# Performance work log

Measured on AMD Instinct MI355X. Metric: run time of the kernel, lower is better.

Reference implementation:

```python
import jax, jax.numpy as jnp
import numpy as np

B, S, H, NH = 2, 2048, 1024, 16
DH = H // NH  # 64

def setup_inputs() -> dict:
    key = jax.random.key(0)
    ks = jax.random.split(key, 6)
    return {
        "hidden_states": jax.random.normal(ks[0], (B, S, H), jnp.float32),
        "attention_mask": jnp.zeros((B, 1, 1, S), jnp.float32),  # additive mask (0 = attend)
        "local_attention_mask": jax.random.randint(ks[1], (B, 1, S, S), 0, 2).astype(jnp.int32),
        "gate_outputs": jax.random.uniform(ks[2], (B, NH, S, 1), jnp.float32),
        "Wq": jax.random.normal(ks[3], (H, H), jnp.float32) * 0.02,
        "bq": jnp.zeros((H,), jnp.float32),
        "Wk": jax.random.normal(ks[4], (H, H), jnp.float32) * 0.02,
        "bk": jnp.zeros((H,), jnp.float32),
        "Wv": jax.random.normal(ks[5], (H, H), jnp.float32) * 0.02,
        "bv": jnp.zeros((H,), jnp.float32),
    }

def _heads(x):
    # [B,S,H] -> [B,NH,S,DH]
    return x.reshape(B, S, NH, DH).transpose(0, 2, 1, 3)

def reference(hidden_states, attention_mask, local_attention_mask, gate_outputs, Wq, bq, Wk, bk, Wv, bv):
    q = _heads(hidden_states @ Wq.T + bq)
    k = _heads(hidden_states @ Wk.T + bk)
    v = _heads(hidden_states @ Wv.T + bv)
    scores = jnp.einsum("bhqd,bhkd->bhqk", q, k) / jnp.sqrt(jnp.float32(DH))
    # global branch (additive mask)
    probs_g = jax.nn.softmax(scores + attention_mask, axis=-1)
    ctx_g = jnp.einsum("bhqk,bhkd->bhqd", probs_g, v)
    # local branch: 0/1 mask -> additive -inf mask
    lmask = (1.0 - local_attention_mask.astype(jnp.float32)) * jnp.finfo(jnp.float32).min
    probs_l = jax.nn.softmax(scores + lmask, axis=-1)
    ctx_l = jnp.einsum("bhqk,bhkd->bhqd", probs_l, v)
    ctx = gate_outputs * ctx_l + (1.0 - gate_outputs) * ctx_g  # [B,NH,S,DH]
    return ctx.transpose(0, 2, 1, 3).reshape(B, S, H)
```

## Files before the change

kernel.cpp:

```cpp
#include <hip/hip_runtime.h>
#include <cstdint>
#include <cstddef>

typedef short short8 __attribute__((ext_vector_type(8)));
typedef short short4v __attribute__((ext_vector_type(4)));
typedef float floatx4 __attribute__((ext_vector_type(4)));
typedef unsigned short ushort4v __attribute__((ext_vector_type(4)));

constexpr int B_ = 2, S_ = 2048, H_ = 1024, NH_ = 16, DH_ = 64;
constexpr int K_ = H_;

__device__ __forceinline__ unsigned short f2bf(float f) {
  unsigned u = __float_as_uint(f);
  u += 0x7fffu + ((u >> 16) & 1u);
  return (unsigned short)(u >> 16);
}

__device__ __forceinline__ unsigned pack2bf(float a, float b) {
  unsigned ua = (__float_as_uint(a) + 0x8000u) >> 16;
  unsigned ub = (__float_as_uint(b) + 0x8000u) & 0xffff0000u;
  return ua | ub;
}

__global__ __launch_bounds__(256) void prep_kernel(
    const float* __restrict__ hs, unsigned short* __restrict__ hbf,
    const float* __restrict__ Wq, const float* __restrict__ Wk, const float* __restrict__ Wv,
    unsigned short* __restrict__ wqb, unsigned short* __restrict__ wkb,
    unsigned short* __restrict__ wvb,
    const int* __restrict__ lm, unsigned long long* __restrict__ bm,
    const float* __restrict__ am, float* __restrict__ ea) {
  const int bid = blockIdx.x, tid = threadIdx.x;
  if (bid < 7168) {
    const float* in;
    unsigned short* out;
    int off;
    if (bid < 4096) { in = hs; out = hbf; off = bid; }
    else {
      int wsel = (bid - 4096) >> 10;
      in = (wsel == 0) ? Wq : (wsel == 1) ? Wk : Wv;
      out = (wsel == 0) ? wqb : (wsel == 1) ? wkb : wvb;
      off = (bid - 4096) & 1023;
    }
    int i = (off * 256 + tid) * 4;
    float4 v = *reinterpret_cast<const float4*>(in + i);
    ushort4v o;
    o.x = f2bf(v.x); o.y = f2bf(v.y); o.z = f2bf(v.z); o.w = f2bf(v.w);
    *reinterpret_cast<ushort4v*>(out + i) = o;
  } else if (bid < 39936) {
    int word = (bid - 7168) * 4 + (tid >> 6);
    int lane = tid & 63;
    unsigned long long bits = __ballot(lm[(size_t)word * 64 + lane] != 0);
    if (lane == 0) bm[word] = bits;
  } else {
    int i = (bid - 39936) * 256 + tid;
    ea[i] = __expf(am[i]);
  }
}

typedef __attribute__((address_space(1))) const void gvoid;
typedef __attribute__((address_space(3))) void lvoid;
__device__ __forceinline__ void async16(const unsigned short* gp, unsigned short* lp) {
  __builtin_amdgcn_global_load_lds((gvoid*)gp, (lvoid*)lp, 16, 0, 0);
}

__global__ __launch_bounds__(256) void gemm_qkv(
    const unsigned short* __restrict__ A,
    const unsigned short* __restrict__ Wq, const unsigned short* __restrict__ Wk,
    const unsigned short* __restrict__ Wv,
    const float* __restrict__ bq, const float* __restrict__ bk, const float* __restrict__ bv,
    unsigned short* __restrict__ qo, unsigned short* __restrict__ ko,
    unsigned short* __restrict__ vo) {
  __shared__ alignas(16) unsigned short As[128 * 32];
  __shared__ alignas(16) unsigned short Bs[128 * 32];
  const int z = blockIdx.z;
  const unsigned short* W = (z == 0) ? Wq : (z == 1) ? Wk : Wv;
  const float* bias = (z == 0) ? bq : (z == 1) ? bk : bv;

  const int m0 = blockIdx.x * 128, n0 = blockIdx.y * 128;
  const int tid = threadIdx.x, lane = tid & 63, wvi = tid >> 6;
  const int wr = wvi >> 1, wc = wvi & 1, quad = lane >> 4, l16 = lane & 15;

  floatx4 zf = {0.f, 0.f, 0.f, 0.f};
  floatx4 acc[4][4];
  for (int i = 0; i < 4; i++)
    for (int j = 0; j < 4; j++) acc[i][j] = zf;

  for (int kk = 0; kk < K_; kk += 32) {
#pragma unroll
    for (int i = 0; i < 2; i++) {
      int cb = wvi * 128 + i * 64;
      int c = cb + lane;
      int row = c >> 2, kc = c & 3;
      async16(A + (size_t)(m0 + row) * K_ + kk + kc * 8, As + cb * 8);
      async16(W + (size_t)(n0 + row) * K_ + kk + kc * 8, Bs + cb * 8);
    }
    __syncthreads();
    short8 af[4], bfr[4];
#pragma unroll
    for (int mf = 0; mf < 4; mf++)
      af[mf] = *reinterpret_cast<const short8*>(&As[(wr * 64 + mf * 16 + l16) * 32 + quad * 8]);
#pragma unroll
    for (int nf = 0; nf < 4; nf++)
      bfr[nf] = *reinterpret_cast<const short8*>(&Bs[(wc * 64 + nf * 16 + l16) * 32 + quad * 8]);
    if (z == 2) {
#pragma unroll
      for (int mf = 0; mf < 4; mf++)
#pragma unroll
        for (int nf = 0; nf < 4; nf++)
          acc[mf][nf] = __builtin_amdgcn_mfma_f32_16x16x32_bf16(af[mf], bfr[nf], acc[mf][nf], 0, 0, 0);
    } else {
#pragma unroll
      for (int mf = 0; mf < 4; mf++)
#pragma unroll
        for (int nf = 0; nf < 4; nf++)
          acc[mf][nf] = __builtin_amdgcn_mfma_f32_16x16x32_bf16(bfr[nf], af[mf], acc[mf][nf], 0, 0, 0);
    }
    __syncthreads();
  }

  if (z == 2) {
#pragma unroll
    for (int mf = 0; mf < 4; mf++) {
      int mbase = m0 + wr * 64 + mf * 16 + quad * 4;
      int b = mbase >> 11, s0 = mbase & 2047;
#pragma unroll
      for (int nf = 0; nf < 4; nf++) {
        int n = n0 + wc * 64 + nf * 16 + l16;
        int h = n >> 6, d = n & 63;
        int bh = b * NH_ + h;
        float bvv = bias[n];
        floatx4 c = acc[mf][nf];
        size_t base = (size_t)bh * 131072 + (s0 >> 6) * 4096 + (d >> 4) * 1024 +
                      ((s0 >> 4) & 3) * 256 + ((s0 >> 2) & 3) * 64 + (d & 15) * 4;
        ushort4v p;
        p.x = f2bf(c[0] + bvv); p.y = f2bf(c[1] + bvv);
        p.z = f2bf(c[2] + bvv); p.w = f2bf(c[3] + bvv);
        *reinterpret_cast<ushort4v*>(&vo[base]) = p;
      }
    }
  } else {
#pragma unroll
    for (int mf = 0; mf < 4; mf++) {
      int s = m0 + wr * 64 + mf * 16 + l16;
      int b = s >> 11;
      int sq = s & 2047;
#pragma unroll
      for (int nf = 0; nf < 4; nf++) {
        int nn = n0 + wc * 64 + nf * 16 + quad * 4;
        int h = nn >> 6, dh = nn & 63;
        int bh = b * NH_ + h;
        float4 b4 = *reinterpret_cast<const float4*>(bias + nn);
        floatx4 c = acc[mf][nf];
        if (z == 0) {
          ushort4v p;
          p.x = f2bf((c[0] + b4.x) * 0.18033688011112042f);
          p.y = f2bf((c[1] + b4.y) * 0.18033688011112042f);
          p.z = f2bf((c[2] + b4.z) * 0.18033688011112042f);
          p.w = f2bf((c[3] + b4.w) * 0.18033688011112042f);
          *reinterpret_cast<ushort4v*>(&qo[((size_t)bh * S_ + sq) * DH_ + dh]) = p;
        } else {
          size_t base = (size_t)bh * 131072 + (sq >> 6) * 4096 + ((sq >> 4) & 3) * 1024 +
                        (dh >> 5) * 512 + ((dh >> 3) & 3) * 128 + (sq & 15) * 8 + (dh & 7);
          ushort4v p;
          p.x = f2bf(c[0] + b4.x); p.y = f2bf(c[1] + b4.y);
          p.z = f2bf(c[2] + b4.z); p.w = f2bf(c[3] + b4.w);
          *reinterpret_cast<ushort4v*>(&ko[base]) = p;
        }
      }
    }
  }
}

__global__ __launch_bounds__(256, 4) void attn_kernel(
    const unsigned short* __restrict__ q,
    const unsigned short* __restrict__ kperm,
    const unsigned short* __restrict__ vperm,
    const float* __restrict__ eam,
    const unsigned long long* __restrict__ bm,
    const float* __restrict__ gate,
    float* __restrict__ out) {
  __shared__ alignas(16) unsigned short Ks[2][4096];
  __shared__ alignas(16) unsigned short Vs[2][4096];

  const int flat = blockIdx.x;
  const int h = (flat & 7) + 8 * ((flat >> 3) & 1);
  const int b = (flat >> 4) & 1;
  const int qt = flat >> 5;
  const int tid = threadIdx.x, lane = tid & 63, wvi = tid >> 6;
  const int quad = lane >> 4, l16 = lane & 15;
  const int bh = b * NH_ + h;
  const int q0 = qt * 64 + wvi * 16;

  const unsigned short* qrow = q + ((size_t)bh * S_ + q0 + l16) * DH_;
  short8 qf0 = *reinterpret_cast<const short8*>(qrow + quad * 8);
  short8 qf1 = *reinterpret_cast<const short8*>(qrow + 32 + quad * 8);

  floatx4 zf = {0.f, 0.f, 0.f, 0.f};
  float psg = 0.f, psl = 0.f;
  floatx4 accg[4], accl[4];
#pragma unroll
  for (int i = 0; i < 4; i++) { accg[i] = zf; accl[i] = zf; }

  const unsigned short* kp = kperm + (size_t)bh * 131072;
  const unsigned short* vp = vperm + (size_t)bh * 131072;
  const float* eamb = eam + (size_t)b * S_;
  const unsigned long long* bmq = bm + ((size_t)b * S_ + q0 + l16) * (S_ / 64);

  const int soA = tid * 8, soB = 2048 + tid * 8;
  const unsigned short* kgA = kp + soA;
  const unsigned short* kgB = kp + soB;
  const unsigned short* vgA = vp + soA;
  const unsigned short* vgB = vp + soB;

  uint4 pk0 = *reinterpret_cast<const uint4*>(kgA);
  uint4 pk1 = *reinterpret_cast<const uint4*>(kgB);
  uint4 pv0 = *reinterpret_cast<const uint4*>(vgA);
  uint4 pv1 = *reinterpret_cast<const uint4*>(vgB);
  *reinterpret_cast<uint4*>(&Ks[0][soA]) = pk0;
  *reinterpret_cast<uint4*>(&Ks[0][soB]) = pk1;
  *reinterpret_cast<uint4*>(&Vs[0][soA]) = pv0;
  *reinterpret_cast<uint4*>(&Vs[0][soB]) = pv1;
  pk0 = *reinterpret_cast<const uint4*>(kgA + 4096);
  pk1 = *reinterpret_cast<const uint4*>(kgB + 4096);
  pv0 = *reinterpret_cast<const uint4*>(vgA + 4096);
  pv1 = *reinterpret_cast<const uint4*>(vgB + 4096);

  for (int kt = 0; kt < S_ / 64; kt++) {
    __syncthreads();
    {
      const int bn = (kt + 1) & 1;
      *reinterpret_cast<uint4*>(&Ks[bn][soA]) = pk0;
      *reinterpret_cast<uint4*>(&Ks[bn][soB]) = pk1;
      *reinterpret_cast<uint4*>(&Vs[bn][soA]) = pv0;
      *reinterpret_cast<uint4*>(&Vs[bn][soB]) = pv1;
    }
    {
      const int tb = ((kt + 2) & 31) * 4096;
      pk0 = *reinterpret_cast<const uint4*>(kgA + tb);
      pk1 = *reinterpret_cast<const uint4*>(kgB + tb);
      pv0 = *reinterpret_cast<const uint4*>(vgA + tb);
      pv1 = *reinterpret_cast<const uint4*>(vgB + tb);
    }
    const int k0 = kt * 64;
    unsigned long long w = bmq[kt];
    float4 ea[4];
#pragma unroll
    for (int t = 0; t < 4; t++)
      ea[t] = *reinterpret_cast<const float4*>(eamb + k0 + t * 16 + quad * 4);

    const unsigned short* Kc = Ks[kt & 1];
    const unsigned short* Vc = Vs[kt & 1];
    floatx4 scT[4];
#pragma unroll
    for (int t = 0; t < 4; t++) {
      const unsigned short* kr = Kc + t * 1024 + lane * 8;
      short8 kf0 = *reinterpret_cast<const short8*>(kr);
      short8 kf1 = *reinterpret_cast<const short8*>(kr + 512);
      scT[t] = __builtin_amdgcn_mfma_f32_16x16x32_bf16(kf0, qf0, zf, 0, 0, 0);
      scT[t] = __builtin_amdgcn_mfma_f32_16x16x32_bf16(kf1, qf1, scT[t], 0, 0, 0);
    }
    int pgf[4][2], plf[4][2];
#pragma unroll
    for (int t = 0; t < 4; t++) {
      unsigned m4 = (unsigned)(w >> (t * 16 + quad * 4)) & 0xFu;
      float e0 = __builtin_amdgcn_exp2f(scT[t][0]);
      float e1 = __builtin_amdgcn_exp2f(scT[t][1]);
      float e2 = __builtin_amdgcn_exp2f(scT[t][2]);
      float e3 = __builtin_amdgcn_exp2f(scT[t][3]);
      float g0 = e0 * ea[t].x, g1 = e1 * ea[t].y, g2 = e2 * ea[t].z, g3 = e3 * ea[t].w;
      psg += (g0 + g1) + (g2 + g3);
      float l0 = (m4 & 1u) ? e0 : 0.f;
      float l1 = (m4 & 2u) ? e1 : 0.f;
      float l2 = (m4 & 4u) ? e2 : 0.f;
      float l3 = (m4 & 8u) ? e3 : 0.f;
      psl += (l0 + l1) + (l2 + l3);
      pgf[t][0] = pack2bf(g0, g1); pgf[t][1] = pack2bf(g2, g3);
      plf[t][0] = pack2bf(l0, l1); plf[t][1] = pack2bf(l2, l3);
    }
#pragma unroll
    for (int d = 0; d < 4; d++) {
#pragma unroll
      for (int t = 0; t < 4; t++) {
        short4v vf = *reinterpret_cast<const short4v*>(Vc + d * 1024 + t * 256 + lane * 4);
        short4v pg = *reinterpret_cast<const short4v*>(&pgf[t][0]);
        short4v pl = *reinterpret_cast<const short4v*>(&plf[t][0]);
        accg[d] = __builtin_amdgcn_mfma_f32_16x16x16bf16_1k(vf, pg, accg[d], 0, 0, 0);
        accl[d] = __builtin_amdgcn_mfma_f32_16x16x16bf16_1k(vf, pl, accl[d], 0, 0, 0);
      }
    }
  }

  float lgf = psg;
  lgf += __shfl_xor(lgf, 16, 64);
  lgf += __shfl_xor(lgf, 32, 64);
  float llf = psl;
  llf += __shfl_xor(llf, 16, 64);
  llf += __shfl_xor(llf, 32, 64);
  const int s = q0 + l16;
  const float g = gate[(size_t)bh * S_ + s];
  const float cg = (1.f - g) / lgf, cl = g / llf;
  float* orow = out + ((size_t)b * S_ + s) * H_ + h * DH_ + quad * 4;
#pragma unroll
  for (int d = 0; d < 4; d++) {
    float4 o;
    o.x = cl * accl[d][0] + cg * accg[d][0];
    o.y = cl * accl[d][1] + cg * accg[d][1];
    o.z = cl * accl[d][2] + cg * accg[d][2];
    o.w = cl * accl[d][3] + cg * accg[d][3];
    *reinterpret_cast<float4*>(orow + d * 16) = o;
  }
}

extern "C" void kernel_launch(void* const* d_in, const int* in_sizes, int n_in,
                              void* d_out, int out_size, void* d_ws, size_t ws_size,
                              hipStream_t stream) {
  (void)in_sizes; (void)n_in; (void)out_size; (void)ws_size;
  const float* hs = (const float*)d_in[0];
  const float* am = (const float*)d_in[1];
  const int* lm = (const int*)d_in[2];
  const float* gate = (const float*)d_in[3];
  const float* Wq = (const float*)d_in[4];
  const float* bq = (const float*)d_in[5];
  const float* Wk = (const float*)d_in[6];
  const float* bk = (const float*)d_in[7];
  const float* Wv = (const float*)d_in[8];
  const float* bv = (const float*)d_in[9];
  float* out = (float*)d_out;

  unsigned short* ws = (unsigned short*)d_ws;
  unsigned short* hbf = ws;
  unsigned short* wqb = hbf + 4194304;
  unsigned short* wkb = wqb + 1048576;
  unsigned short* wvb = wkb + 1048576;
  unsigned short* qb = wvb + 1048576;
  unsigned short* kb = qb + 4194304;
  unsigned short* vtb = kb + 4194304;
  unsigned long long* bmp = (unsigned long long*)(vtb + 4194304);
  float* eamp = (float*)(bmp + 131072);

  prep_kernel<<<39952, 256, 0, stream>>>(hs, hbf, Wq, Wk, Wv, wqb, wkb, wvb, lm, bmp, am, eamp);
  gemm_qkv<<<dim3(32, 8, 3), 256, 0, stream>>>(hbf, wqb, wkb, wvb, bq, bk, bv, qb, kb, vtb);
  attn_kernel<<<dim3(1024), 256, 0, stream>>>(qb, kb, vtb, eamp, bmp, gate, out);
}
```

Measured before the change: 267.4 us.

## Use 16x16x32 MFMA for PV product with permuted K/V layouts

Switches the P·V product from 16x16x16 to 16x16x32 bf16 MFMAs, which halves the MFMA instruction count. To make the P fragments line up with the wider K dimension, the K and V global layouts written by the projection kernel are re-permuted, and the mask bits and additive-mask loads are regrouped to match. Software bf16 packing is replaced by the hardware v_cvt_pk_bf16_f32 instruction. This depends on the permutations matching the MFMA operand layout exactly, and the new conversion may round differently.

```diff
diff --git a/kernel.cpp b/kernel.cpp
--- a/kernel.cpp
+++ b/kernel.cpp
@@ -6,6 +6,7 @@
 typedef short short4v __attribute__((ext_vector_type(4)));
 typedef float floatx4 __attribute__((ext_vector_type(4)));
 typedef unsigned short ushort4v __attribute__((ext_vector_type(4)));
+typedef unsigned int uintx4 __attribute__((ext_vector_type(4)));
 
 constexpr int B_ = 2, S_ = 2048, H_ = 1024, NH_ = 16, DH_ = 64;
 constexpr int K_ = H_;
@@ -16,10 +17,10 @@
   return (unsigned short)(u >> 16);
 }
 
-__device__ __forceinline__ unsigned pack2bf(float a, float b) {
-  unsigned ua = (__float_as_uint(a) + 0x8000u) >> 16;
-  unsigned ub = (__float_as_uint(b) + 0x8000u) & 0xffff0000u;
-  return ua | ub;
+__device__ __forceinline__ unsigned cvtpk(float a, float b) {
+  unsigned r;
+  asm("v_cvt_pk_bf16_f32 %0, %1, %2" : "=v"(r) : "v"(a), "v"(b));
+  return r;
 }
 
 __global__ __launch_bounds__(256) void prep_kernel(
@@ -123,6 +124,7 @@
     for (int mf = 0; mf < 4; mf++) {
       int mbase = m0 + wr * 64 + mf * 16 + quad * 4;
       int b = mbase >> 11, s0 = mbase & 2047;
+      int kl = s0 & 63;
 #pragma unroll
       for (int nf = 0; nf < 4; nf++) {
         int n = n0 + wc * 64 + nf * 16 + l16;
@@ -131,7 +133,7 @@
         float bvv = bias[n];
         floatx4 c = acc[mf][nf];
         size_t base = (size_t)bh * 131072 + (s0 >> 6) * 4096 + (d >> 4) * 1024 +
-                      ((s0 >> 4) & 3) * 256 + ((s0 >> 2) & 3) * 64 + (d & 15) * 4;
+                      (kl >> 5) * 512 + ((kl >> 3) & 3) * 128 + (d & 15) * 8 + (kl & 7);
         ushort4v p;
         p.x = f2bf(c[0] + bvv); p.y = f2bf(c[1] + bvv);
         p.z = f2bf(c[2] + bvv); p.w = f2bf(c[3] + bvv);
@@ -159,8 +161,11 @@
           p.w = f2bf((c[3] + b4.w) * 0.18033688011112042f);
           *reinterpret_cast<ushort4v*>(&qo[((size_t)bh * S_ + sq) * DH_ + dh]) = p;
         } else {
-          size_t base = (size_t)bh * 131072 + (sq >> 6) * 4096 + ((sq >> 4) & 3) * 1024 +
-                        (dh >> 5) * 512 + ((dh >> 3) & 3) * 128 + (sq & 15) * 8 + (dh & 7);
+          int kl = sq & 63;
+          int t = ((kl >> 4) & 2) | ((kl >> 2) & 1);
+          int rr = ((kl >> 1) & 12) | (kl & 3);
+          size_t base = (size_t)bh * 131072 + (sq >> 6) * 4096 + t * 1024 +
+                        (dh >> 5) * 512 + ((dh >> 3) & 3) * 128 + rr * 8 + (dh & 7);
           ushort4v p;
           p.x = f2bf(c[0] + b4.x); p.y = f2bf(c[1] + b4.y);
           p.z = f2bf(c[2] + b4.z); p.w = f2bf(c[3] + b4.w);
@@ -190,6 +195,7 @@
   const int quad = lane >> 4, l16 = lane & 15;
   const int bh = b * NH_ + h;
   const int q0 = qt * 64 + wvi * 16;
+  const int quad8 = quad * 8;
 
   const unsigned short* qrow = q + ((size_t)bh * S_ + q0 + l16) * DH_;
   short8 qf0 = *reinterpret_cast<const short8*>(qrow + quad * 8);
@@ -242,11 +248,13 @@
       pv1 = *reinterpret_cast<const uint4*>(vgB + tb);
     }
     const int k0 = kt * 64;
-    unsigned long long w = bmq[kt];
-    float4 ea[4];
-#pragma unroll
-    for (int t = 0; t < 4; t++)
-      ea[t] = *reinterpret_cast<const float4*>(eamb + k0 + t * 16 + quad * 4);
+    uint2 wv = *reinterpret_cast<const uint2*>(&bmq[kt]);
+    unsigned wq0 = wv.x >> quad8;
+    unsigned wq1 = wv.y >> quad8;
+    float4 ea0 = *reinterpret_cast<const float4*>(eamb + k0 + quad8);
+    float4 ea1 = *reinterpret_cast<const float4*>(eamb + k0 + 4 + quad8);
+    float4 ea2 = *reinterpret_cast<const float4*>(eamb + k0 + 32 + quad8);
+    float4 ea3 = *reinterpret_cast<const float4*>(eamb + k0 + 36 + quad8);
 
     const unsigned short* Kc = Ks[kt & 1];
     const unsigned short* Vc = Vs[kt & 1];
@@ -259,34 +267,43 @@
       scT[t] = __builtin_amdgcn_mfma_f32_16x16x32_bf16(kf0, qf0, zf, 0, 0, 0);
       scT[t] = __builtin_amdgcn_mfma_f32_16x16x32_bf16(kf1, qf1, scT[t], 0, 0, 0);
     }
-    int pgf[4][2], plf[4][2];
+    uintx4 fgv[2], flv[2];
 #pragma unroll
     for (int t = 0; t < 4; t++) {
-      unsigned m4 = (unsigned)(w >> (t * 16 + quad * 4)) & 0xFu;
-      float e0 = __builtin_amdgcn_exp2f(scT[t][0]);
-      float e1 = __builtin_amdgcn_exp2f(scT[t][1]);
-      float e2 = __builtin_amdgcn_exp2f(scT[t][2]);
-      float e3 = __builtin_amdgcn_exp2f(scT[t][3]);
-      float g0 = e0 * ea[t].x, g1 = e1 * ea[t].y, g2 = e2 * ea[t].z, g3 = e3 * ea[t].w;
+      const int T = t >> 1, tau = t & 1;
+      floatx4 sc = scT[t];
+      unsigned wq = T ? wq1 : wq0;
+      float4 ea = (t == 0) ? ea0 : (t == 1) ? ea1 : (t == 2) ? ea2 : ea3;
+      unsigned m4 = (wq >> (tau * 4)) & 0xFu;
+      float e0 = __builtin_amdgcn_exp2f(sc[0]);
+      float e1 = __builtin_amdgcn_exp2f(sc[1]);
+      float e2 = __builtin_amdgcn_exp2f(sc[2]);
+      float e3 = __builtin_amdgcn_exp2f(sc[3]);
+      float g0 = e0 * ea.x, g1 = e1 * ea.y, g2 = e2 * ea.z, g3 = e3 * ea.w;
       psg += (g0 + g1) + (g2 + g3);
       float l0 = (m4 & 1u) ? e0 : 0.f;
       float l1 = (m4 & 2u) ? e1 : 0.f;
       float l2 = (m4 & 4u) ? e2 : 0.f;
       float l3 = (m4 & 8u) ? e3 : 0.f;
       psl += (l0 + l1) + (l2 + l3);
-      pgf[t][0] = pack2bf(g0, g1); pgf[t][1] = pack2bf(g2, g3);
-      plf[t][0] = pack2bf(l0, l1); plf[t][1] = pack2bf(l2, l3);
-    }
+      fgv[T][tau * 2]     = cvtpk(g0, g1);
+      fgv[T][tau * 2 + 1] = cvtpk(g2, g3);
+      flv[T][tau * 2]     = cvtpk(l0, l1);
+      flv[T][tau * 2 + 1] = cvtpk(l2, l3);
+    }
+    short8 FG0 = __builtin_bit_cast(short8, fgv[0]);
+    short8 FG1 = __builtin_bit_cast(short8, fgv[1]);
+    short8 FL0 = __builtin_bit_cast(short8, flv[0]);
+    short8 FL1 = __builtin_bit_cast(short8, flv[1]);
 #pragma unroll
     for (int d = 0; d < 4; d++) {
-#pragma unroll
-      for (int t = 0; t < 4; t++) {
-        short4v vf = *reinterpret_cast<const short4v*>(Vc + d * 1024 + t * 256 + lane * 4);
-        short4v pg = *reinterpret_cast<const short4v*>(&pgf[t][0]);
-        short4v pl = *reinterpret_cast<const short4v*>(&plf[t][0]);
-        accg[d] = __builtin_amdgcn_mfma_f32_16x16x16bf16_1k(vf, pg, accg[d], 0, 0, 0);
-        accl[d] = __builtin_amdgcn_mfma_f32_16x16x16bf16_1k(vf, pl, accl[d], 0, 0, 0);
-      }
+      const unsigned short* vb = Vc + d * 1024 + lane * 8;
+      short8 v0 = *reinterpret_cast<const short8*>(vb);
+      short8 v1 = *reinterpret_cast<const short8*>(vb + 512);
+      accg[d] = __builtin_amdgcn_mfma_f32_16x16x32_bf16(v0, FG0, accg[d], 0, 0, 0);
+      accl[d] = __builtin_amdgcn_mfma_f32_16x16x32_bf16(v0, FL0, accl[d], 0, 0, 0);
+      accg[d] = __builtin_amdgcn_mfma_f32_16x16x32_bf16(v1, FG1, accg[d], 0, 0, 0);
+      accl[d] = __builtin_amdgcn_mfma_f32_16x16x32_bf16(v1, FL1, accl[d], 0, 0, 0);
     }
   }
 
```

Measured after the change: 229.8 us. 1.16x faster.
